# Optimization experiments

Hardware: AMD Instinct MI355X
Metric: run time of the kernel (lower is better)

Reference implementation:

```python
import jax, jax.numpy as jnp
import numpy as np

B, S, D = 2, 2048, 2048
H, HKV, HD = 32, 8, 64
G = H // HKV  # num_key_value_groups


def setup_inputs() -> dict:
    key = jax.random.key(0)
    ks = jax.random.split(key, 9)
    sc = 0.02
    return {
        "x": jax.random.normal(ks[0], (B, S, D), jnp.float32),
        "wq": jax.random.normal(ks[1], (H * HD, D), jnp.float32) * sc,
        "bq": jax.random.normal(ks[2], (H * HD,), jnp.float32) * sc,
        "wk": jax.random.normal(ks[3], (HKV * HD, D), jnp.float32) * sc,
        "bk": jax.random.normal(ks[4], (HKV * HD,), jnp.float32) * sc,
        "wv": jax.random.normal(ks[5], (HKV * HD, D), jnp.float32) * sc,
        "bv": jax.random.normal(ks[6], (HKV * HD,), jnp.float32) * sc,
        "wo": jax.random.normal(ks[7], (D, H * HD), jnp.float32) * sc,
        "bo": jax.random.normal(ks[8], (D,), jnp.float32) * sc,
    }


def reference(x, wq, bq, wk, bk, wv, bv, wo, bo):
    b, s, _ = x.shape
    # fused-QKV-style projections (nn.Linear: x @ W.T + b)
    q = (jnp.einsum("bsd,ed->bse", x, wq) + bq).reshape(b, s, H, HD)
    k = (jnp.einsum("bsd,ed->bse", x, wk) + bk).reshape(b, s, HKV, HD)
    v = (jnp.einsum("bsd,ed->bse", x, wv) + bv).reshape(b, s, HKV, HD)
    # (B, Hkv, G, S, hd): grouped query heads share a KV head — same math as
    # repeat_kv (expand+flatten) without materializing the expanded KV tensor
    q = q.transpose(0, 2, 1, 3).reshape(b, HKV, G, s, HD)
    k = k.transpose(0, 2, 1, 3)  # (B, Hkv, S, hd)
    v = v.transpose(0, 2, 1, 3)
    scale = 1.0 / jnp.sqrt(jnp.asarray(HD, x.dtype))
    scores = jnp.einsum("bkgqd,bktd->bkgqt", q, k) * scale  # (B,Hkv,G,S,S)
    causal = jnp.tril(jnp.ones((s, s), bool))
    scores = jnp.where(causal, scores, jnp.asarray(-jnp.inf, scores.dtype))
    probs = jax.nn.softmax(scores, axis=-1)
    o = jnp.einsum("bkgqt,bktd->bkgqd", probs, v)  # (B,Hkv,G,S,hd)
    o = o.reshape(b, H, s, HD).transpose(0, 2, 1, 3).reshape(b, s, H * HD)
    return jnp.einsum("bse,de->bsd", o, wo) + bo
```

## Files before the change

kernel.cpp:

```cpp
#include <hip/hip_runtime.h>
#include <hip/hip_bf16.h>
#include <cmath>

#define B_   2
#define S_   2048
#define D_   2048
#define H_   32
#define HKV_ 8
#define HD_  64

using bf16 = __hip_bfloat16;
typedef __bf16    bf16x8 __attribute__((ext_vector_type(8)));
typedef float     floatx4 __attribute__((ext_vector_type(4)));
typedef _Float16  half4 __attribute__((ext_vector_type(4)));

#if __has_builtin(__builtin_amdgcn_exp2f)
#define EXP2(x) __builtin_amdgcn_exp2f(x)
#else
#define EXP2(x) exp2f(x)
#endif

#define QSCALE 0.18033688011112042f

__device__ inline void async16(const void* g, void* l) {
  __builtin_amdgcn_global_load_lds(
      (const __attribute__((address_space(1))) void*)g,
      (__attribute__((address_space(3))) void*)l, 16, 0, 0);
}

#define MFMA32B(a, b, c) __builtin_amdgcn_mfma_f32_16x16x32_bf16((a), (b), (c), 0, 0, 0)
#define MFMA16H(a, b, c) __builtin_amdgcn_mfma_f32_16x16x16f16((a), (b), (c), 0, 0, 0)

__global__ void f2b_all(const float* __restrict__ x,  const float* __restrict__ wq,
                        const float* __restrict__ wk, const float* __restrict__ wv,
                        const float* __restrict__ wo,
                        bf16* __restrict__ xb,  bf16* __restrict__ wqb,
                        bf16* __restrict__ wkb, bf16* __restrict__ wvb,
                        bf16* __restrict__ wob) {
  const int i = blockIdx.x * blockDim.x + threadIdx.x;
  const float* src; bf16* dst; int off; float scale = 1.0f;
  if (i < 1048576)      { src = x;  dst = xb;  off = 0; }
  else if (i < 1572864) { src = wq; dst = wqb; off = 1048576; scale = QSCALE; }
  else if (i < 1703936) { src = wk; dst = wkb; off = 1572864; }
  else if (i < 1835008) { src = wv; dst = wvb; off = 1703936; }
  else                  { src = wo; dst = wob; off = 1835008; }
  const int j = i - off;
  float4 a  = ((const float4*)src)[2 * j];
  float4 b2 = ((const float4*)src)[2 * j + 1];
  alignas(16) bf16 t[8];
  t[0] = __float2bfloat16(a.x * scale);  t[1] = __float2bfloat16(a.y * scale);
  t[2] = __float2bfloat16(a.z * scale);  t[3] = __float2bfloat16(a.w * scale);
  t[4] = __float2bfloat16(b2.x * scale); t[5] = __float2bfloat16(b2.y * scale);
  t[6] = __float2bfloat16(b2.z * scale); t[7] = __float2bfloat16(b2.w * scale);
  ((uint4*)dst)[j] = *(const uint4*)t;
}

template <int MODE, typename OutT>
__device__ inline void gemm_body(const bf16* __restrict__ Ag, const bf16* __restrict__ Bg,
                                 const float* __restrict__ bias, float bscale,
                                 OutT* __restrict__ C, int Ncol, int K, int bm, int colb,
                                 bf16* As, bf16* Bs) {
  const int tid  = threadIdx.x;
  const int wid  = tid >> 6, lane = tid & 63;
  const int lm   = lane & 15, quad = lane >> 4;
  const int wm   = (wid >> 1) * 64, wn = (wid & 1) * 64;

  floatx4 acc[4][4] = {};

  const int l0 = tid * 8;
  const int r0 = l0 >> 5, c0 = l0 & 31;
  const int r1 = r0 + 64;

  for (int k0 = 0; k0 < K; k0 += 32) {
    async16(Ag + (size_t)r0 * K + k0 + c0, &As[l0]);
    async16(Ag + (size_t)r1 * K + k0 + c0, &As[l0 + 2048]);
    async16(Bg + (size_t)r0 * K + k0 + c0, &Bs[l0]);
    async16(Bg + (size_t)r1 * K + k0 + c0, &Bs[l0 + 2048]);
    asm volatile("s_waitcnt vmcnt(0)" ::: "memory");
    __syncthreads();

    bf16x8 aF[4], bF[4];
#pragma unroll
    for (int mi = 0; mi < 4; ++mi)
      aF[mi] = *(const bf16x8*)&As[(wm + mi * 16 + lm) * 32 + quad * 8];
#pragma unroll
    for (int ni = 0; ni < 4; ++ni)
      bF[ni] = *(const bf16x8*)&Bs[(wn + ni * 16 + lm) * 32 + quad * 8];
#pragma unroll
    for (int mi = 0; mi < 4; ++mi)
#pragma unroll
      for (int ni = 0; ni < 4; ++ni) {
        acc[mi][ni] = MFMA32B(bF[ni], aF[mi], acc[mi][ni]);
      }
    __syncthreads();
  }

#pragma unroll
  for (int mi = 0; mi < 4; ++mi) {
    const int row = bm * 128 + wm + mi * 16 + lm;
#pragma unroll
    for (int ni = 0; ni < 4; ++ni) {
      const int col0 = colb + wn + ni * 16 + quad * 4;
      float4 bv4 = *(const float4*)&bias[col0];
      float4 o4;
      o4.x = acc[mi][ni][0] + bv4.x; o4.y = acc[mi][ni][1] + bv4.y;
      o4.z = acc[mi][ni][2] + bv4.z; o4.w = acc[mi][ni][3] + bv4.w;
      *(float4*)&((float*)C)[(size_t)row * Ncol + col0] = o4;
    }
  }
}

__global__ __launch_bounds__(256, 2)
void gemm_o(const bf16* __restrict__ A, const bf16* __restrict__ Bm,
            const float* __restrict__ bias, float* __restrict__ C,
            int Ncol, int K) {
  __shared__ bf16 As[128 * 32];
  __shared__ bf16 Bs[128 * 32];
  const int bn = blockIdx.x, bm = blockIdx.y;
  gemm_body<1, float>(A + (size_t)bm * 128 * K, Bm + (size_t)bn * 128 * K, bias, 1.0f,
                      C, Ncol, K, bm, bn * 128, As, Bs);
}

template <int MODE>
__device__ __forceinline__ void qkv8_body(
    const bf16* __restrict__ Ag, const bf16* __restrict__ Bg,
    const float* __restrict__ bias, float bscale,
    bf16* __restrict__ outB, _Float16* __restrict__ outV,
    int Ncol, int colb, int bm, bf16* L) {
  constexpr int NT = D_ / 64;
  const int tid = threadIdx.x;
  const int wid = tid >> 6, lane = tid & 63;
  const int lm = lane & 15, quad = lane >> 4;
  const int wm = wid >> 2, wn = wid & 3;

  const int cOff = (quad * 8) ^ (((lm >> 3) & 1) << 4);
  const bf16* LA0 = L + (wm * 128 + lm) * 32 + cOff;
  const bf16* LB0 = L + 8192 + (wn * 64 + lm) * 32 + cOff;

  const int r0 = tid >> 2;
  const int csrc = ((tid & 3) * 8) ^ (((tid >> 5) & 1) << 4);
  const bf16* Asrc = Ag + (size_t)r0 * D_ + csrc;
  const bf16* Bsrc = Bg + (size_t)r0 * D_ + csrc;
  bf16* Ld = L + tid * 8;

  floatx4 acc[8][4] = {};

#define BARX() { asm volatile("" ::: "memory"); __builtin_amdgcn_s_barrier(); \
                 asm volatile("" ::: "memory"); }
#define LGKM0() asm volatile("s_waitcnt lgkmcnt(0)" ::: "memory")
#define STG_A(tt, kk, DB) { const size_t ko = (size_t)(tt) * 64 + (kk) * 32;   \
    async16(Asrc + ko,                   (DB) + (kk) * 16384);                 \
    async16(Asrc + ko + (size_t)128 * D_, (DB) + (kk) * 16384 + 4096); }
#define STG_B(tt, kk, DB) { const size_t ko = (size_t)(tt) * 64 + (kk) * 32;   \
    async16(Bsrc + ko,                   (DB) + 8192 + (kk) * 16384);          \
    async16(Bsrc + ko + (size_t)128 * D_, (DB) + 8192 + (kk) * 16384 + 4096); }

  STG_A(0, 0, Ld); STG_B(0, 0, Ld); STG_A(0, 1, Ld); STG_B(0, 1, Ld);
  STG_A(1, 0, Ld + 32768); STG_B(1, 0, Ld + 32768);
  asm volatile("s_waitcnt vmcnt(8)" ::: "memory");
  BARX();

  auto tile = [&](int t, const int BUF) __attribute__((always_inline)) {
    const bf16* LA = LA0 + BUF;
    const bf16* LB = LB0 + BUF;
    bf16* SD  = Ld + BUF;
    bf16* SDo = Ld + (BUF ^ 32768);
    const bool s1 = (t + 1) < NT, s2 = (t + 2) < NT;
    bf16x8 aF[4], bF[4];

#pragma unroll
    for (int i = 0; i < 4; ++i) aF[i] = *(const bf16x8*)(LA + i * 512);
#pragma unroll
    for (int i = 0; i < 4; ++i) bF[i] = *(const bf16x8*)(LB + i * 512);
    if (s1) STG_A(t + 1, 1, SDo);
    BARX(); LGKM0();
    __builtin_amdgcn_s_setprio(1);
#pragma unroll
    for (int mi = 0; mi < 4; ++mi)
#pragma unroll
      for (int ni = 0; ni < 4; ++ni) {
        if constexpr (MODE == 2) acc[mi][ni] = MFMA32B(aF[mi], bF[ni], acc[mi][ni]);
        else                     acc[mi][ni] = MFMA32B(bF[ni], aF[mi], acc[mi][ni]);
      }
    __builtin_amdgcn_s_setprio(0);
    BARX();

#pragma unroll
    for (int i = 0; i < 4; ++i) aF[i] = *(const bf16x8*)(LA + (i + 4) * 512);
    if (s1) STG_B(t + 1, 1, SDo);
    BARX(); LGKM0();
    __builtin_amdgcn_s_setprio(1);
#pragma unroll
    for (int mi = 0; mi < 4; ++mi)
#pragma unroll
      for (int ni = 0; ni < 4; ++ni) {
        if constexpr (MODE == 2) acc[mi + 4][ni] = MFMA32B(aF[mi], bF[ni], acc[mi + 4][ni]);
        else                     acc[mi + 4][ni] = MFMA32B(bF[ni], aF[mi], acc[mi + 4][ni]);
      }
    __builtin_amdgcn_s_setprio(0);
    if (s1) { asm volatile("s_waitcnt vmcnt(8)" ::: "memory"); }
    else    { asm volatile("s_waitcnt vmcnt(0)" ::: "memory"); }
    BARX();

#pragma unroll
    for (int i = 0; i < 4; ++i) aF[i] = *(const bf16x8*)(LA + 16384 + i * 512);
#pragma unroll
    for (int i = 0; i < 4; ++i) bF[i] = *(const bf16x8*)(LB + 16384 + i * 512);
    if (s2) STG_A(t + 2, 0, SD);
    BARX(); LGKM0();
    __builtin_amdgcn_s_setprio(1);
#pragma unroll
    for (int mi = 0; mi < 4; ++mi)
#pragma unroll
      for (int ni = 0; ni < 4; ++ni) {
        if constexpr (MODE == 2) acc[mi][ni] = MFMA32B(aF[mi], bF[ni], acc[mi][ni]);
        else                     acc[mi][ni] = MFMA32B(bF[ni], aF[mi], acc[mi][ni]);
      }
    __builtin_amdgcn_s_setprio(0);
    BARX();

#pragma unroll
    for (int i = 0; i < 4; ++i) aF[i] = *(const bf16x8*)(LA + 16384 + (i + 4) * 512);
    if (s2) STG_B(t + 2, 0, SD);
    BARX(); LGKM0();
    __builtin_amdgcn_s_setprio(1);
#pragma unroll
    for (int mi = 0; mi < 4; ++mi)
#pragma unroll
      for (int ni = 0; ni < 4; ++ni) {
        if constexpr (MODE == 2) acc[mi + 4][ni] = MFMA32B(aF[mi], bF[ni], acc[mi + 4][ni]);
        else                     acc[mi + 4][ni] = MFMA32B(bF[ni], aF[mi], acc[mi + 4][ni]);
      }
    __builtin_amdgcn_s_setprio(0);
    if (s2)      { asm volatile("s_waitcnt vmcnt(8)" ::: "memory"); }
    else if (s1) { asm volatile("s_waitcnt vmcnt(4)" ::: "memory"); }
    BARX();
  };

  for (int t = 0; t < NT; t += 2) { tile(t, 0); tile(t + 1, 32768); }

#undef BARX
#undef LGKM0
#undef STG_A
#undef STG_B

  const int rowb = bm * 256 + wm * 128;
  if constexpr (MODE == 0) {
#pragma unroll
    for (int mi = 0; mi < 8; ++mi) {
      const int row = rowb + mi * 16 + lm;
#pragma unroll
      for (int ni = 0; ni < 4; ++ni) {
        const int col0 = colb + wn * 64 + ni * 16 + quad * 4;
        float4 bv4 = *(const float4*)&bias[col0];
        alignas(8) bf16 t4[4];
#pragma unroll
        for (int r = 0; r < 4; ++r)
          t4[r] = __float2bfloat16(acc[mi][ni][r] + ((const float*)&bv4)[r] * bscale);
        *(uint2*)&outB[(size_t)row * Ncol + col0] = *(const uint2*)t4;
      }
    }
  } else {
#pragma unroll
    for (int mi = 0; mi < 8; ++mi) {
      const int rowg = rowb + mi * 16 + quad * 4;
      const int b    = rowg >> 11, s = rowg & 2047;
      const int tl   = s >> 6, kvin = s & 63;
      const int kc   = kvin >> 4, qd = (kvin >> 2) & 3;
#pragma unroll
      for (int ni = 0; ni < 4; ++ni) {
        const int col = colb + wn * 64 + ni * 16 + lm;
        const float bv = bias[col];
        const int kvh = col >> 6, hd = col & 63;
        const int nh = hd >> 4, lmw = hd & 15;
        const size_t base = ((size_t)((b * 8 + kvh) * 32 + tl) << 12) +
                            (((kc * 4 + nh) * 4 + qd) << 6) + (lmw << 2);
        alignas(8) _Float16 t4[4];
#pragma unroll
        for (int r = 0; r < 4; ++r)
          t4[r] = (_Float16)(acc[mi][ni][r] + bv);
        *(uint2*)&outV[base] = *(const uint2*)t4;
      }
    }
  }
}

__global__ __launch_bounds__(512, 2)
void gemm_qkv8(const bf16* __restrict__ xb,
               const bf16* __restrict__ wq, const bf16* __restrict__ wk,
               const bf16* __restrict__ wv,
               const float* __restrict__ bq, const float* __restrict__ bk,
               const float* __restrict__ bv,
               bf16* __restrict__ Qo, bf16* __restrict__ Ko,
               _Float16* __restrict__ VG) {
  __shared__ bf16 L[65536];
  const int id  = blockIdx.x;
  const int swz = (id & 7) * 24 + (id >> 3);
  const int bm  = swz / 12, bn = swz % 12;
  const bf16* Ag = xb + (size_t)bm * 256 * D_;
  if (bn < 8) {
    qkv8_body<0>(Ag, wq + (size_t)bn * 256 * D_, bq, QSCALE, Qo, nullptr,
                 H_ * HD_, bn * 256, bm, L);
  } else if (bn < 10) {
    qkv8_body<0>(Ag, wk + (size_t)(bn - 8) * 256 * D_, bk, 1.0f, Ko, nullptr,
                 HKV_ * HD_, (bn - 8) * 256, bm, L);
  } else {
    qkv8_body<2>(Ag, wv + (size_t)(bn - 10) * 256 * D_, bv, 1.0f, nullptr, VG,
                 HKV_ * HD_, (bn - 10) * 256, bm, L);
  }
}

__global__ __launch_bounds__(256, 4)
void attn_kernel(const bf16* __restrict__ Q, const bf16* __restrict__ K,
                 const _Float16* __restrict__ VG, bf16* __restrict__ O) {
  const int tid = threadIdx.x;
  const int wid = tid >> 6, lane = tid & 63;
  const int lm = lane & 15, quad = lane >> 4;

  const int n   = blockIdx.y * 64 + blockIdx.x;
  const int x3  = n & 7, b1 = (n >> 3) & 1;
  const int pair = n >> 4;
  const int grp  = x3 * 2 + b1;
  const int b    = grp >> 3, kvh = grp & 7;
  const int head = kvh * 4 + wid;

  const int hi = 127 - pair, lo = pair;
  const int nt_hi = (hi >> 2) + 1;
  const int nt_lo = (lo >> 2) + 1;

  __shared__ bf16     Ks[2 * 64 * 64];
  __shared__ _Float16 Vs[2 * 64 * 64];

  const int tb[2] = {hi * 16, lo * 16};

  bf16x8 qf[2][2];
#pragma unroll
  for (int tt = 0; tt < 2; ++tt) {
    const size_t qg = ((size_t)(b * S_ + tb[tt] + lm)) * (H_ * HD_) + head * HD_;
#pragma unroll
    for (int kf = 0; kf < 2; ++kf)
      qf[tt][kf] = *(const bf16x8*)&Q[qg + kf * 32 + quad * 8];
  }

  half4 onesh;
#pragma unroll
  for (int j = 0; j < 4; ++j) onesh[j] = (_Float16)1.0f;

  floatx4 o_acc[2][4] = {};
  floatx4 lacc[2] = {};

  const int tr = tid >> 2;
  const int tc = (tid & 3) * 8;

  auto stage = [&](int t, int buf) {
#pragma unroll
    for (int c = 0; c < 2; ++c) {
      async16(&K[(size_t)(b * S_ + t * 64 + tr) * (HKV_ * HD_) + kvh * HD_ + c * 32 + tc],
              &Ks[buf * 4096 + c * 2048 + tid * 8]);
      async16(&VG[((size_t)(grp * 32 + t) << 12) + c * 2048 + tid * 8],
              &Vs[buf * 4096 + c * 2048 + tid * 8]);
    }
  };

  stage(0, 0);

  for (int t = 0; t < nt_hi; ++t) {
    const int cur = t & 1;
    asm volatile("s_waitcnt vmcnt(0)" ::: "memory");
    __syncthreads();
    if (t + 1 < nt_hi) stage(t + 1, cur ^ 1);

    const bf16*     Kb = &Ks[cur * 4096];
    const _Float16* Vb = &Vs[cur * 4096];
    const int t0 = t * 64;
    const int nact = (t < nt_lo) ? 2 : 1;

    int kcmax[2], kcross[2];
#pragma unroll
    for (int tt = 0; tt < 2; ++tt) {
      const int rel = tb[tt] + 15 - t0;
      kcmax[tt]  = (tt < nact) ? ((rel >> 4) >= 3 ? 4 : (rel >> 4) + 1) : 0;
      kcross[tt] = rel >> 4;
    }

    half4 pb[2][4];
#pragma unroll
    for (int kc = 0; kc < 4; ++kc) {
      if (kc >= kcmax[0]) break;
      bf16x8 kb0 = *(const bf16x8*)&Kb[(kc * 16 + lm) * 32 + quad * 8];
      bf16x8 kb1 = *(const bf16x8*)&Kb[2048 + (kc * 16 + lm) * 32 + quad * 8];
#pragma unroll
      for (int tt = 0; tt < 2; ++tt) {
        if (kc >= kcmax[tt]) continue;
        floatx4 sT = {};
        sT = MFMA32B(kb0, qf[tt][0], sT);
        sT = MFMA32B(kb1, qf[tt][1], sT);
        half4 pk;
        if (kc == kcross[tt]) {
          const int qrel = tb[tt] + lm - t0;
#pragma unroll
          for (int r = 0; r < 4; ++r) {
            float p = (kc * 16 + quad * 4 + r > qrel) ? 0.f : EXP2(sT[r]);
            pk[r] = (_Float16)p;
          }
        } else {
#pragma unroll
          for (int r = 0; r < 4; ++r) pk[r] = (_Float16)EXP2(sT[r]);
        }
        pb[tt][kc] = pk;
      }
    }

#pragma unroll
    for (int tt = 0; tt < 2; ++tt) {
      if (kcmax[tt] == 0) continue;
      half4 ps = pb[tt][0];
      if (kcmax[tt] > 1) ps += pb[tt][1];
      if (kcmax[tt] > 2) ps += pb[tt][2];
      if (kcmax[tt] > 3) ps += pb[tt][3];
      lacc[tt] = MFMA16H(onesh, ps, lacc[tt]);
    }

#pragma unroll
    for (int kc = 0; kc < 4; ++kc) {
      if (kc >= kcmax[0]) break;
#pragma unroll
      for (int nh = 0; nh < 4; ++nh) {
        half4 va = *(const half4*)&Vb[((kc * 4 + nh) * 4 + quad) * 64 + lm * 4];
#pragma unroll
        for (int tt = 0; tt < 2; ++tt)
          if (kc < kcmax[tt]) o_acc[tt][nh] = MFMA16H(va, pb[tt][kc], o_acc[tt][nh]);
      }
    }
  }

#pragma unroll
  for (int tt = 0; tt < 2; ++tt) {
    const float rl = 1.f / lacc[tt][0];
    const size_t rowg = (size_t)(b * S_ + tb[tt] + lm);
#pragma unroll
    for (int nh = 0; nh < 4; ++nh) {
      alignas(8) bf16 tmp[4];
#pragma unroll
      for (int r = 0; r < 4; ++r)
        tmp[r] = __float2bfloat16(o_acc[tt][nh][r] * rl);
      *(uint2*)&O[rowg * (H_ * HD_) + head * HD_ + nh * 16 + quad * 4] = *(uint2*)tmp;
    }
  }
}

extern "C" void kernel_launch(void* const* d_in, const int* in_sizes, int n_in,
                              void* d_out, int out_size, void* d_ws, size_t ws_size,
                              hipStream_t stream) {
  (void)in_sizes; (void)n_in; (void)out_size; (void)ws_size;
  const float* x  = (const float*)d_in[0];
  const float* wq = (const float*)d_in[1];
  const float* bq = (const float*)d_in[2];
  const float* wk = (const float*)d_in[3];
  const float* bk = (const float*)d_in[4];
  const float* wv = (const float*)d_in[5];
  const float* bv = (const float*)d_in[6];
  const float* wo = (const float*)d_in[7];
  const float* bo = (const float*)d_in[8];
  float* out = (float*)d_out;

  const int M = B_ * S_;
  const int E = H_ * HD_;
  const int EKV = HKV_ * HD_;

  char* ws = (char*)d_ws;
  size_t off = 0;
  auto alloc = [&](size_t bytes) {
    char* p = ws + off;
    off += (bytes + 255) & ~(size_t)255;
    return p;
  };
  bf16* xb  = (bf16*)alloc((size_t)M * D_ * 2);
  bf16* wqb = (bf16*)alloc((size_t)E * D_ * 2);
  bf16* wkb = (bf16*)alloc((size_t)EKV * D_ * 2);
  bf16* wvb = (bf16*)alloc((size_t)EKV * D_ * 2);
  bf16* wob = (bf16*)alloc((size_t)D_ * E * 2);
  bf16* Qb  = (bf16*)alloc((size_t)M * E * 2);
  bf16* Kb  = (bf16*)alloc((size_t)M * EKV * 2);
  _Float16* VG = (_Float16*)alloc((size_t)M * EKV * 2);
  bf16* Ob  = (bf16*)alloc((size_t)M * E * 2);

  f2b_all<<<9216, 256, 0, stream>>>(x, wq, wk, wv, wo, xb, wqb, wkb, wvb, wob);

  gemm_qkv8<<<dim3(192), dim3(512), 0, stream>>>(xb, wqb, wkb, wvb, bq, bk, bv,
                                                 Qb, Kb, VG);

  attn_kernel<<<dim3(64, 16), 256, 0, stream>>>(Qb, Kb, VG, Ob);

  gemm_o<<<dim3(D_ / 128, M / 128), 256, 0, stream>>>(Ob, wob, bo, out, D_, D_);
}
```

Before: 303.2 us.

## Retile fused QKV GEMM to 128x384 tiles over concatenated weights

Concatenates Wq, Wk and Wv into one contiguous bf16 buffer. The fused QKV GEMM now uses 128x384 output tiles (256 blocks) instead of 256x256 tiles (192 blocks), with each block's columns spanning Q, K and V regions that are split in the epilogue. The aim is better wave balance across the CUs, since 256 blocks fill the machine more evenly than 192. In exchange, the V epilogue writes scalar fp16 values instead of packed ones, and the taller-narrower tile changes how much of each operand is reused.

```diff
diff --git a/kernel.cpp b/kernel.cpp
--- a/kernel.cpp
+++ b/kernel.cpp
@@ -55,10 +55,9 @@
   ((uint4*)dst)[j] = *(const uint4*)t;
 }
 
-template <int MODE, typename OutT>
 __device__ inline void gemm_body(const bf16* __restrict__ Ag, const bf16* __restrict__ Bg,
-                                 const float* __restrict__ bias, float bscale,
-                                 OutT* __restrict__ C, int Ncol, int K, int bm, int colb,
+                                 const float* __restrict__ bias,
+                                 float* __restrict__ C, int Ncol, int K, int bm, int colb,
                                  bf16* As, bf16* Bs) {
   const int tid  = threadIdx.x;
   const int wid  = tid >> 6, lane = tid & 63;
@@ -89,9 +88,8 @@
 #pragma unroll
     for (int mi = 0; mi < 4; ++mi)
 #pragma unroll
-      for (int ni = 0; ni < 4; ++ni) {
+      for (int ni = 0; ni < 4; ++ni)
         acc[mi][ni] = MFMA32B(bF[ni], aF[mi], acc[mi][ni]);
-      }
     __syncthreads();
   }
 
@@ -105,7 +103,7 @@
       float4 o4;
       o4.x = acc[mi][ni][0] + bv4.x; o4.y = acc[mi][ni][1] + bv4.y;
       o4.z = acc[mi][ni][2] + bv4.z; o4.w = acc[mi][ni][3] + bv4.w;
-      *(float4*)&((float*)C)[(size_t)row * Ncol + col0] = o4;
+      *(float4*)&C[(size_t)row * Ncol + col0] = o4;
     }
   }
 }
@@ -117,46 +115,54 @@
   __shared__ bf16 As[128 * 32];
   __shared__ bf16 Bs[128 * 32];
   const int bn = blockIdx.x, bm = blockIdx.y;
-  gemm_body<1, float>(A + (size_t)bm * 128 * K, Bm + (size_t)bn * 128 * K, bias, 1.0f,
-                      C, Ncol, K, bm, bn * 128, As, Bs);
-}
-
-template <int MODE>
-__device__ __forceinline__ void qkv8_body(
-    const bf16* __restrict__ Ag, const bf16* __restrict__ Bg,
-    const float* __restrict__ bias, float bscale,
-    bf16* __restrict__ outB, _Float16* __restrict__ outV,
-    int Ncol, int colb, int bm, bf16* L) {
+  gemm_body(A + (size_t)bm * 128 * K, Bm + (size_t)bn * 128 * K, bias,
+            C, Ncol, K, bm, bn * 128, As, Bs);
+}
+
+__global__ __launch_bounds__(512, 2)
+void gemm_qkv8(const bf16* __restrict__ xb, const bf16* __restrict__ Wcat,
+               const float* __restrict__ bq, const float* __restrict__ bk,
+               const float* __restrict__ bv,
+               bf16* __restrict__ Qo, bf16* __restrict__ Ko,
+               _Float16* __restrict__ VG) {
   constexpr int NT = D_ / 64;
+  __shared__ bf16 L[65536];
+
+  const int id = blockIdx.x;
+  const int bn = id & 7;
+  const int bm = id >> 3;
+
   const int tid = threadIdx.x;
   const int wid = tid >> 6, lane = tid & 63;
   const int lm = lane & 15, quad = lane >> 4;
   const int wm = wid >> 2, wn = wid & 3;
 
   const int cOff = (quad * 8) ^ (((lm >> 3) & 1) << 4);
-  const bf16* LA0 = L + (wm * 128 + lm) * 32 + cOff;
-  const bf16* LB0 = L + 8192 + (wn * 64 + lm) * 32 + cOff;
+  const bf16* LA0 = L + (wm * 64 + lm) * 32 + cOff;
+  const bf16* LB0 = L + 8192 + (wn * 96 + lm) * 32 + cOff;
 
   const int r0 = tid >> 2;
   const int csrc = ((tid & 3) * 8) ^ (((tid >> 5) & 1) << 4);
-  const bf16* Asrc = Ag + (size_t)r0 * D_ + csrc;
-  const bf16* Bsrc = Bg + (size_t)r0 * D_ + csrc;
+  const bf16* Asrc = xb   + (size_t)(bm * 128 + r0) * D_ + csrc;
+  const bf16* Bs0  = Wcat + (size_t)(bn * 384 + r0) * D_ + csrc;
+  const bf16* Bs1  = Bs0 + (size_t)128 * D_;
+  const bf16* Bs2  = Bs0 + (size_t)256 * D_;
   bf16* Ld = L + tid * 8;
 
-  floatx4 acc[8][4] = {};
+  floatx4 acc[4][6] = {};
 
 #define BARX() { asm volatile("" ::: "memory"); __builtin_amdgcn_s_barrier(); \
                  asm volatile("" ::: "memory"); }
 #define LGKM0() asm volatile("s_waitcnt lgkmcnt(0)" ::: "memory")
-#define STG_A(tt, kk, DB) { const size_t ko = (size_t)(tt) * 64 + (kk) * 32;   \
-    async16(Asrc + ko,                   (DB) + (kk) * 16384);                 \
-    async16(Asrc + ko + (size_t)128 * D_, (DB) + (kk) * 16384 + 4096); }
-#define STG_B(tt, kk, DB) { const size_t ko = (size_t)(tt) * 64 + (kk) * 32;   \
-    async16(Bsrc + ko,                   (DB) + 8192 + (kk) * 16384);          \
-    async16(Bsrc + ko + (size_t)128 * D_, (DB) + 8192 + (kk) * 16384 + 4096); }
-
-  STG_A(0, 0, Ld); STG_B(0, 0, Ld); STG_A(0, 1, Ld); STG_B(0, 1, Ld);
-  STG_A(1, 0, Ld + 32768); STG_B(1, 0, Ld + 32768);
+#define STG_A(tt, hh, DB)  async16(Asrc + (tt) * 64 + (hh) * 32, (DB) + (hh) * 4096)
+#define STG_B0(tt, hh, DB) async16(Bs0  + (tt) * 64 + (hh) * 32, (DB) + 8192 + (hh) * 12288)
+#define STG_B1(tt, hh, DB) async16(Bs1  + (tt) * 64 + (hh) * 32, (DB) + 8192 + (hh) * 12288 + 4096)
+#define STG_B2(tt, hh, DB) async16(Bs2  + (tt) * 64 + (hh) * 32, (DB) + 8192 + (hh) * 12288 + 8192)
+
+  STG_A(0, 0, Ld); STG_B0(0, 0, Ld); STG_B1(0, 0, Ld); STG_B2(0, 0, Ld);
+  STG_A(0, 1, Ld); STG_B0(0, 1, Ld); STG_B1(0, 1, Ld); STG_B2(0, 1, Ld);
+  STG_A(1, 0, Ld + 32768); STG_B0(1, 0, Ld + 32768);
+  STG_B1(1, 0, Ld + 32768); STG_B2(1, 0, Ld + 32768);
   asm volatile("s_waitcnt vmcnt(8)" ::: "memory");
   BARX();
 
@@ -166,74 +172,67 @@
     bf16* SD  = Ld + BUF;
     bf16* SDo = Ld + (BUF ^ 32768);
     const bool s1 = (t + 1) < NT, s2 = (t + 2) < NT;
-    bf16x8 aF[4], bF[4];
+    bf16x8 aF[4], bF[3];
 
 #pragma unroll
     for (int i = 0; i < 4; ++i) aF[i] = *(const bf16x8*)(LA + i * 512);
 #pragma unroll
-    for (int i = 0; i < 4; ++i) bF[i] = *(const bf16x8*)(LB + i * 512);
-    if (s1) STG_A(t + 1, 1, SDo);
+    for (int i = 0; i < 3; ++i) bF[i] = *(const bf16x8*)(LB + i * 512);
+    if (s1) { STG_A(t + 1, 1, SDo); STG_B0(t + 1, 1, SDo); }
     BARX(); LGKM0();
     __builtin_amdgcn_s_setprio(1);
 #pragma unroll
     for (int mi = 0; mi < 4; ++mi)
 #pragma unroll
-      for (int ni = 0; ni < 4; ++ni) {
-        if constexpr (MODE == 2) acc[mi][ni] = MFMA32B(aF[mi], bF[ni], acc[mi][ni]);
-        else                     acc[mi][ni] = MFMA32B(bF[ni], aF[mi], acc[mi][ni]);
-      }
+      for (int ni = 0; ni < 3; ++ni)
+        acc[mi][ni] = MFMA32B(bF[ni], aF[mi], acc[mi][ni]);
     __builtin_amdgcn_s_setprio(0);
     BARX();
 
 #pragma unroll
-    for (int i = 0; i < 4; ++i) aF[i] = *(const bf16x8*)(LA + (i + 4) * 512);
-    if (s1) STG_B(t + 1, 1, SDo);
+    for (int i = 0; i < 3; ++i) bF[i] = *(const bf16x8*)(LB + (i + 3) * 512);
+    if (s1) { STG_B1(t + 1, 1, SDo); STG_B2(t + 1, 1, SDo); }
     BARX(); LGKM0();
     __builtin_amdgcn_s_setprio(1);
 #pragma unroll
     for (int mi = 0; mi < 4; ++mi)
 #pragma unroll
-      for (int ni = 0; ni < 4; ++ni) {
-        if constexpr (MODE == 2) acc[mi + 4][ni] = MFMA32B(aF[mi], bF[ni], acc[mi + 4][ni]);
-        else                     acc[mi + 4][ni] = MFMA32B(bF[ni], aF[mi], acc[mi + 4][ni]);
-      }
+      for (int ni = 0; ni < 3; ++ni)
+        acc[mi][ni + 3] = MFMA32B(bF[ni], aF[mi], acc[mi][ni + 3]);
     __builtin_amdgcn_s_setprio(0);
     if (s1) { asm volatile("s_waitcnt vmcnt(8)" ::: "memory"); }
     else    { asm volatile("s_waitcnt vmcnt(0)" ::: "memory"); }
     BARX();
 
 #pragma unroll
-    for (int i = 0; i < 4; ++i) aF[i] = *(const bf16x8*)(LA + 16384 + i * 512);
-#pragma unroll
-    for (int i = 0; i < 4; ++i) bF[i] = *(const bf16x8*)(LB + 16384 + i * 512);
-    if (s2) STG_A(t + 2, 0, SD);
+    for (int i = 0; i < 4; ++i) aF[i] = *(const bf16x8*)(LA + 4096 + i * 512);
+#pragma unroll
+    for (int i = 0; i < 3; ++i) bF[i] = *(const bf16x8*)(LB + 12288 + i * 512);
+    if (s2) { STG_A(t + 2, 0, SD); STG_B0(t + 2, 0, SD); }
     BARX(); LGKM0();
     __builtin_amdgcn_s_setprio(1);
 #pragma unroll
     for (int mi = 0; mi < 4; ++mi)
 #pragma unroll
-      for (int ni = 0; ni < 4; ++ni) {
-        if constexpr (MODE == 2) acc[mi][ni] = MFMA32B(aF[mi], bF[ni], acc[mi][ni]);
-        else                     acc[mi][ni] = MFMA32B(bF[ni], aF[mi], acc[mi][ni]);
-      }
+      for (int ni = 0; ni < 3; ++ni)
+        acc[mi][ni] = MFMA32B(bF[ni], aF[mi], acc[mi][ni]);
     __builtin_amdgcn_s_setprio(0);
     BARX();
 
 #pragma unroll
-    for (int i = 0; i < 4; ++i) aF[i] = *(const bf16x8*)(LA + 16384 + (i + 4) * 512);
-    if (s2) STG_B(t + 2, 0, SD);
+    for (int i = 0; i < 3; ++i) bF[i] = *(const bf16x8*)(LB + 12288 + (i + 3) * 512);
+    if (s2) { STG_B1(t + 2, 0, SD); STG_B2(t + 2, 0, SD); }
     BARX(); LGKM0();
     __builtin_amdgcn_s_setprio(1);
 #pragma unroll
     for (int mi = 0; mi < 4; ++mi)
 #pragma unroll
-      for (int ni = 0; ni < 4; ++ni) {
-        if constexpr (MODE == 2) acc[mi + 4][ni] = MFMA32B(aF[mi], bF[ni], acc[mi + 4][ni]);
-        else                     acc[mi + 4][ni] = MFMA32B(bF[ni], aF[mi], acc[mi + 4][ni]);
-      }
+      for (int ni = 0; ni < 3; ++ni)
+        acc[mi][ni + 3] = MFMA32B(bF[ni], aF[mi], acc[mi][ni + 3]);
     __builtin_amdgcn_s_setprio(0);
     if (s2)      { asm volatile("s_waitcnt vmcnt(8)" ::: "memory"); }
     else if (s1) { asm volatile("s_waitcnt vmcnt(4)" ::: "memory"); }
+    else         { asm volatile("s_waitcnt vmcnt(0)" ::: "memory"); }
     BARX();
   };
 
@@ -242,71 +241,48 @@
 #undef BARX
 #undef LGKM0
 #undef STG_A
-#undef STG_B
-
-  const int rowb = bm * 256 + wm * 128;
-  if constexpr (MODE == 0) {
-#pragma unroll
-    for (int mi = 0; mi < 8; ++mi) {
-      const int row = rowb + mi * 16 + lm;
-#pragma unroll
-      for (int ni = 0; ni < 4; ++ni) {
-        const int col0 = colb + wn * 64 + ni * 16 + quad * 4;
-        float4 bv4 = *(const float4*)&bias[col0];
+#undef STG_B0
+#undef STG_B1
+#undef STG_B2
+
+#pragma unroll
+  for (int mi = 0; mi < 4; ++mi) {
+    const int row = bm * 128 + wm * 64 + mi * 16 + lm;
+#pragma unroll
+    for (int ni = 0; ni < 6; ++ni) {
+      const int colf = bn * 384 + wn * 96 + ni * 16;
+      const int col0 = colf + quad * 4;
+      if (colf < 2048) {
+        float4 bv4 = *(const float4*)&bq[col0];
         alignas(8) bf16 t4[4];
 #pragma unroll
         for (int r = 0; r < 4; ++r)
-          t4[r] = __float2bfloat16(acc[mi][ni][r] + ((const float*)&bv4)[r] * bscale);
-        *(uint2*)&outB[(size_t)row * Ncol + col0] = *(const uint2*)t4;
+          t4[r] = __float2bfloat16(acc[mi][ni][r] + ((const float*)&bv4)[r] * QSCALE);
+        *(uint2*)&Qo[(size_t)row * (H_ * HD_) + col0] = *(const uint2*)t4;
+      } else if (colf < 2560) {
+        const int ck = col0 - 2048;
+        float4 bv4 = *(const float4*)&bk[ck];
+        alignas(8) bf16 t4[4];
+#pragma unroll
+        for (int r = 0; r < 4; ++r)
+          t4[r] = __float2bfloat16(acc[mi][ni][r] + ((const float*)&bv4)[r]);
+        *(uint2*)&Ko[(size_t)row * (HKV_ * HD_) + ck] = *(const uint2*)t4;
+      } else {
+        const int cv = col0 - 2560;
+        const int kvh = cv >> 6, hd = cv & 63;
+        const int nh = hd >> 4;
+        const int bb = row >> 11, s2 = row & 2047;
+        const int tl = s2 >> 6, kvin = s2 & 63;
+        const int kc = kvin >> 4, qd = (kvin >> 2) & 3, j = kvin & 3;
+        const size_t base = ((size_t)((bb * 8 + kvh) * 32 + tl) << 12) +
+                            (((kc * 4 + nh) * 4 + qd) << 6) + j;
+        float4 bv4 = *(const float4*)&bv[cv];
+#pragma unroll
+        for (int r = 0; r < 4; ++r)
+          VG[base + (size_t)(quad * 4 + r) * 4] =
+              (_Float16)(acc[mi][ni][r] + ((const float*)&bv4)[r]);
       }
     }
-  } else {
-#pragma unroll
-    for (int mi = 0; mi < 8; ++mi) {
-      const int rowg = rowb + mi * 16 + quad * 4;
-      const int b    = rowg >> 11, s = rowg & 2047;
-      const int tl   = s >> 6, kvin = s & 63;
-      const int kc   = kvin >> 4, qd = (kvin >> 2) & 3;
-#pragma unroll
-      for (int ni = 0; ni < 4; ++ni) {
-        const int col = colb + wn * 64 + ni * 16 + lm;
-        const float bv = bias[col];
-        const int kvh = col >> 6, hd = col & 63;
-        const int nh = hd >> 4, lmw = hd & 15;
-        const size_t base = ((size_t)((b * 8 + kvh) * 32 + tl) << 12) +
-                            (((kc * 4 + nh) * 4 + qd) << 6) + (lmw << 2);
-        alignas(8) _Float16 t4[4];
-#pragma unroll
-        for (int r = 0; r < 4; ++r)
-          t4[r] = (_Float16)(acc[mi][ni][r] + bv);
-        *(uint2*)&outV[base] = *(const uint2*)t4;
-      }
-    }
-  }
-}
-
-__global__ __launch_bounds__(512, 2)
-void gemm_qkv8(const bf16* __restrict__ xb,
-               const bf16* __restrict__ wq, const bf16* __restrict__ wk,
-               const bf16* __restrict__ wv,
-               const float* __restrict__ bq, const float* __restrict__ bk,
-               const float* __restrict__ bv,
-               bf16* __restrict__ Qo, bf16* __restrict__ Ko,
-               _Float16* __restrict__ VG) {
-  __shared__ bf16 L[65536];
-  const int id  = blockIdx.x;
-  const int swz = (id & 7) * 24 + (id >> 3);
-  const int bm  = swz / 12, bn = swz % 12;
-  const bf16* Ag = xb + (size_t)bm * 256 * D_;
-  if (bn < 8) {
-    qkv8_body<0>(Ag, wq + (size_t)bn * 256 * D_, bq, QSCALE, Qo, nullptr,
-                 H_ * HD_, bn * 256, bm, L);
-  } else if (bn < 10) {
-    qkv8_body<0>(Ag, wk + (size_t)(bn - 8) * 256 * D_, bk, 1.0f, Ko, nullptr,
-                 HKV_ * HD_, (bn - 8) * 256, bm, L);
-  } else {
-    qkv8_body<2>(Ag, wv + (size_t)(bn - 10) * 256 * D_, bv, 1.0f, nullptr, VG,
-                 HKV_ * HD_, (bn - 10) * 256, bm, L);
   }
 }
 
@@ -475,19 +451,21 @@
     off += (bytes + 255) & ~(size_t)255;
     return p;
   };
-  bf16* xb  = (bf16*)alloc((size_t)M * D_ * 2);
-  bf16* wqb = (bf16*)alloc((size_t)E * D_ * 2);
-  bf16* wkb = (bf16*)alloc((size_t)EKV * D_ * 2);
-  bf16* wvb = (bf16*)alloc((size_t)EKV * D_ * 2);
-  bf16* wob = (bf16*)alloc((size_t)D_ * E * 2);
-  bf16* Qb  = (bf16*)alloc((size_t)M * E * 2);
-  bf16* Kb  = (bf16*)alloc((size_t)M * EKV * 2);
+  bf16* xb   = (bf16*)alloc((size_t)M * D_ * 2);
+  bf16* Wcat = (bf16*)alloc((size_t)(E + 2 * EKV) * D_ * 2);
+  bf16* wob  = (bf16*)alloc((size_t)D_ * E * 2);
+  bf16* Qb   = (bf16*)alloc((size_t)M * E * 2);
+  bf16* Kb   = (bf16*)alloc((size_t)M * EKV * 2);
   _Float16* VG = (_Float16*)alloc((size_t)M * EKV * 2);
-  bf16* Ob  = (bf16*)alloc((size_t)M * E * 2);
+  bf16* Ob   = (bf16*)alloc((size_t)M * E * 2);
+
+  bf16* wqb = Wcat;
+  bf16* wkb = Wcat + (size_t)E * D_;
+  bf16* wvb = Wcat + (size_t)(E + EKV) * D_;
 
   f2b_all<<<9216, 256, 0, stream>>>(x, wq, wk, wv, wo, xb, wqb, wkb, wvb, wob);
 
-  gemm_qkv8<<<dim3(192), dim3(512), 0, stream>>>(xb, wqb, wkb, wvb, bq, bk, bv,
+  gemm_qkv8<<<dim3(256), dim3(512), 0, stream>>>(xb, Wcat, bq, bk, bv,
                                                  Qb, Kb, VG);
 
   attn_kernel<<<dim3(64, 16), 256, 0, stream>>>(Qb, Kb, VG, Ob);
```

Result: faster. 285.0 us (-6.0%).
